# Optimization experiments

Hardware: AMD Instinct MI355X
Metric: run time of the kernel (lower is better)

Reference implementation:

```python
import jax, jax.numpy as jnp
import numpy as np

B = 8192          # batch of agents
K = 4             # max_neighbors
NUM_LANES = 12
LANE_F = 4        # obs_dim // num_lanes = 48 // 12
HEADS = 4
OUT = 32          # gat_output_dim per head
EMB = HEADS * OUT # 128, gat_per_lane_output / intersection emb dim
HID = 64          # graphsage_hidden_dim
GRU_H = 32        # gru_hidden_dim
ALPHA = 0.2       # leaky relu slope

# Lane cooperation: lanes of the same approach (4 approaches x 3 lanes) cooperate.
_blk = np.kron(np.eye(4), np.ones((3, 3))).astype(np.float32)
LANE_COOP = jnp.asarray(_blk)
LANE_CONF = jnp.asarray(1.0 - _blk)


def _gat_stream(x, W, a_src, a_dst, adj):
    # x: [N, 12, 4]; W: [H, 4, O]; a_*: [H, O]; adj: [12, 12]
    Wh = jnp.einsum('nlf,hfo->nhlo', x, W)                      # [N,H,12,O]
    e_s = jnp.einsum('nhlo,ho->nhl', Wh, a_src)
    e_d = jnp.einsum('nhlo,ho->nhl', Wh, a_dst)
    e = jax.nn.leaky_relu(e_s[..., :, None] + e_d[..., None, :], ALPHA)  # [N,H,12,12]
    e = jnp.where(adj[None, None] > 0, e, jnp.float32(-1e9))
    att = jax.nn.softmax(e, axis=-1)
    out = jnp.einsum('nhij,nhjo->niho', att, Wh)                # [N,12,H,O]
    return jax.nn.elu(out.reshape(out.shape[0], NUM_LANES, EMB))


def _gru_final(xs, Wih, Whh, bih, bhh):
    # xs: [K, B, HID] -> final hidden [B, GRU_H], torch GRU gate convention (r,z,n)
    def step(h, x):
        gi = x @ Wih + bih
        gh = h @ Whh + bhh
        i_r, i_z, i_n = jnp.split(gi, 3, axis=-1)
        h_r, h_z, h_n = jnp.split(gh, 3, axis=-1)
        r = jax.nn.sigmoid(i_r + h_r)
        z = jax.nn.sigmoid(i_z + h_z)
        n = jnp.tanh(i_n + r * h_n)
        return (1.0 - z) * n + z * h, None
    h0 = jnp.zeros((xs.shape[1], Whh.shape[0]), xs.dtype)
    hT, _ = jax.lax.scan(step, h0, xs)
    return hT


def setup_inputs() -> dict:
    key = jax.random.key(0)
    ks = jax.random.split(key, 24)
    rn = lambda k, s: (jax.random.normal(k, s, jnp.float32) * 0.1)
    z = lambda n: jnp.zeros((n,), jnp.float32)
    return {
        'self_features': jax.random.normal(ks[0], (B, 48), jnp.float32),
        'neighbor_features': jax.random.normal(ks[1], (B, K, 48), jnp.float32),
        'neighbor_mask': (jax.random.uniform(ks[2], (B, K)) > 0.25).astype(jnp.float32),
        'neighbor_directions': jax.random.randint(ks[3], (B, K), 0, 4).astype(jnp.float32) * 0.25,
        # dual-stream GAT params
        'W_coop': rn(ks[4], (HEADS, LANE_F, OUT)), 'a_src_coop': rn(ks[5], (HEADS, OUT)), 'a_dst_coop': rn(ks[6], (HEADS, OUT)),
        'W_conf': rn(ks[7], (HEADS, LANE_F, OUT)), 'a_src_conf': rn(ks[8], (HEADS, OUT)), 'a_dst_conf': rn(ks[9], (HEADS, OUT)),
        'W_fuse': rn(ks[10], (2 * EMB, EMB)), 'b_fuse': z(EMB),
        # GraphSAGE neighbor projection (+1 for direction feature)
        'W_proj': rn(ks[11], (EMB + 1, HID)), 'b_proj': z(HID),
        # BiGRU (fwd/bwd), torch layout transposed: Wih [HID,3H], Whh [H,3H]
        'Wih_f': rn(ks[12], (HID, 3 * GRU_H)), 'Whh_f': rn(ks[13], (GRU_H, 3 * GRU_H)), 'bih_f': z(3 * GRU_H), 'bhh_f': z(3 * GRU_H),
        'Wih_b': rn(ks[14], (HID, 3 * GRU_H)), 'Whh_b': rn(ks[15], (GRU_H, 3 * GRU_H)), 'bih_b': z(3 * GRU_H), 'bhh_b': z(3 * GRU_H),
        # combine self + BiGRU summary -> network embedding
        'W_out': rn(ks[16], (EMB + 2 * GRU_H, HID)), 'b_out': z(HID),
    }


def reference(self_features, neighbor_features, neighbor_mask, neighbor_directions,
              W_coop, a_src_coop, a_dst_coop, W_conf, a_src_conf, a_dst_conf,
              W_fuse, b_fuse, W_proj, b_proj,
              Wih_f, Whh_f, bih_f, bhh_f, Wih_b, Whh_b, bih_b, bhh_b,
              W_out, b_out):
    Bc, Kc = neighbor_features.shape[:2]
    # run dual-stream GAT on self + all neighbors in one batch of small lane graphs
    allx = jnp.concatenate([self_features[:, None, :], neighbor_features], axis=1)
    allx = allx.reshape(Bc * (Kc + 1), NUM_LANES, LANE_F)
    coop = _gat_stream(allx, W_coop, a_src_coop, a_dst_coop, LANE_COOP)
    conf = _gat_stream(allx, W_conf, a_src_conf, a_dst_conf, LANE_CONF)
    fused = jax.nn.elu(jnp.concatenate([coop, conf], axis=-1) @ W_fuse + b_fuse)  # [N,12,128]
    emb = fused.mean(axis=1).reshape(Bc, Kc + 1, EMB)  # mean pool over lanes
    self_emb = emb[:, 0]          # [B,128]
    nbr_emb = emb[:, 1:]          # [B,K,128]
    # GraphSAGE projection of neighbors (direction-aware), masked
    nbr_in = jnp.concatenate([nbr_emb, neighbor_directions[..., None]], axis=-1)
    x = jax.nn.relu(nbr_in @ W_proj + b_proj) * neighbor_mask[..., None]  # [B,K,HID]
    xs = jnp.swapaxes(x, 0, 1)    # [K,B,HID]
    h_f = _gru_final(xs, Wih_f, Whh_f, bih_f, bhh_f)
    h_b = _gru_final(xs[::-1], Wih_b, Whh_b, bih_b, bhh_b)
    net = jax.nn.relu(jnp.concatenate([self_emb, h_f, h_b], axis=-1) @ W_out + b_out)  # [B,64]
    return jnp.concatenate([self_emb, net], axis=-1)  # [B,192]
```

## Files before the change

kernel.cpp:

```cpp
#include <hip/hip_runtime.h>
#include <math.h>

typedef short short8 __attribute__((ext_vector_type(8)));
typedef float f32x4  __attribute__((ext_vector_type(4)));
typedef unsigned short u16x4 __attribute__((ext_vector_type(4)));

__device__ __forceinline__ unsigned short f2b(float f) {
  union { float f; unsigned int u; } x; x.f = f;
  return (unsigned short)((x.u + 0x7FFFu + ((x.u >> 16) & 1u)) >> 16);
}
__device__ __forceinline__ float b2f_u(unsigned short u) {
  union { unsigned int u; float f; } x; x.u = ((unsigned int)u) << 16;
  return x.f;
}
__device__ __forceinline__ float sigm(float x) { return 1.f / (1.f + __expf(-x)); }

__global__ __launch_bounds__(256) void prepack_kernel(
    const float* __restrict__ Wf,
    const float* __restrict__ Wc, const float* __restrict__ Wn,
    const float* __restrict__ as_c, const float* __restrict__ ad_c,
    const float* __restrict__ as_n, const float* __restrict__ ad_n,
    const float* __restrict__ Wproj,
    const float* __restrict__ Wih_f, const float* __restrict__ Wih_b,
    const float* __restrict__ Wout,
    const float* __restrict__ Whh_f, const float* __restrict__ Whh_b,
    unsigned short* __restrict__ fragB,
    unsigned short* __restrict__ fragWB,
    float* __restrict__ Wa,
    unsigned short* __restrict__ fragP,
    unsigned short* __restrict__ fragIH,
    unsigned short* __restrict__ fragO,
    unsigned short* __restrict__ fragHH)
{
  int e = blockIdx.x * 256 + threadIdx.x;
  unsigned short tmp[8];
  if (e < 4096) {
    int kb = e >> 9, tile = (e >> 6) & 7, lane = e & 63;
    int n = tile * 16 + (lane & 15);
    int kbase = kb * 32 + (lane >> 4) * 8;
#pragma unroll
    for (int j = 0; j < 8; j++) tmp[j] = f2b(Wf[(kbase + j) * 128 + n]);
    *(short8*)(fragB + e * 8) = *(short8*)tmp;
  } else if (e < 5120) {
    int i = e - 4096;
    int s = i >> 9, tile = (i >> 6) & 7, lane = i & 63;
    int c15 = lane & 15, quad = lane >> 4;
    int n = tile * 16 + c15;
    int h = n >> 5, o = n & 31;
    const float* W = s ? Wn : Wc;
#pragma unroll
    for (int j = 0; j < 8; j++) {
      int k = quad * 8 + j;
      tmp[j] = ((k >> 2) == h) ? f2b(W[h * 128 + (k & 3) * 32 + o])
                               : (unsigned short)0;
    }
    *(short8*)(fragWB + i * 8) = *(short8*)tmp;
  } else if (e < 5184) {
    int i = e - 5120;
    int s = i >> 5, d = (i >> 4) & 1, h = (i >> 2) & 3, f = i & 3;
    const float* W = s ? Wn : Wc;
    const float* a = s ? (d ? ad_n : as_n) : (d ? ad_c : as_c);
    float acc = 0.f;
#pragma unroll
    for (int o = 0; o < 32; o++) acc += W[h * 128 + f * 32 + o] * a[h * 32 + o];
    Wa[i] = acc;
  } else if (e < 6208) {
    int i = e - 5184;
    int kb = i >> 8, nt = (i >> 6) & 3, lane = i & 63;
    int c15 = lane & 15, quad = lane >> 4;
#pragma unroll
    for (int j = 0; j < 8; j++)
      tmp[j] = f2b(Wproj[(kb * 32 + quad * 8 + j) * 64 + nt * 16 + c15]);
    *(short8*)(fragP + i * 8) = *(short8*)tmp;
  } else if (e < 7744) {
    int i = e - 6208;
    int d = (i >= 768), r = i - d * 768;
    int kb = r / 384, nt = (r >> 6) % 6, lane = r & 63;
    int c15 = lane & 15, quad = lane >> 4;
    const float* W = d ? Wih_b : Wih_f;
#pragma unroll
    for (int j = 0; j < 8; j++)
      tmp[j] = f2b(W[(kb * 32 + quad * 8 + j) * 96 + nt * 16 + c15]);
    *(short8*)(fragIH + i * 8) = *(short8*)tmp;
  } else if (e < 9280) {
    int r = e - 7744;
    int kb = r >> 8, nt = (r >> 6) & 3, lane = r & 63;
    int c15 = lane & 15, quad = lane >> 4;
#pragma unroll
    for (int j = 0; j < 8; j++)
      tmp[j] = f2b(Wout[(kb * 32 + quad * 8 + j) * 64 + nt * 16 + c15]);
    *(short8*)(fragO + r * 8) = *(short8*)tmp;
  } else if (e < 10048) {
    int i = e - 9280;
    int d = i / 384, r = i - d * 384;
    int nt = r >> 6, lane = r & 63;
    int c15 = lane & 15, quad = lane >> 4;
    const float* W = d ? Whh_b : Whh_f;
#pragma unroll
    for (int j = 0; j < 8; j++)
      tmp[j] = f2b(W[(quad * 8 + j) * 96 + nt * 16 + c15]);
    *(short8*)(fragHH + i * 8) = *(short8*)tmp;
  }
}

__global__ __launch_bounds__(256) void gat_fuse_kernel(
    const float* __restrict__ self_f, const float* __restrict__ nbr_f,
    const float* __restrict__ Wa,
    const unsigned short* __restrict__ fragWB,
    const unsigned short* __restrict__ fragB,
    const float* __restrict__ b_fuse,
    float* __restrict__ emb)
{
  const int tid = threadIdx.x;
  const int w = tid >> 6, lane = tid & 63, c15 = lane & 15, quad = lane >> 4;
  const int n0 = blockIdx.x * 2;
  const int ws = w & 1;
  const int wn = w >> 1;

  __shared__ __align__(16) float sxf[2][12][4];
  __shared__ float sWa[64];
  __shared__ float sed[2][2][4][12];
  __shared__ __align__(16) unsigned short sA[2][2][16][24];
  __shared__ __align__(16) unsigned short scatb[2][16][268];
  __shared__ float sbias[128];

  if (tid < 128) sbias[tid] = b_fuse[tid];
  if (tid < 64) sWa[tid] = Wa[tid];
  if (tid < 96) {
    int nd = tid / 48, f = tid - nd * 48;
    int nn = n0 + nd, b = nn / 5, slot = nn - b * 5;
    float v = (slot == 0) ? self_f[b * 48 + f]
                          : nbr_f[(b * 4 + slot - 1) * 48 + f];
    sxf[nd][f >> 2][f & 3] = v;
  }
  __syncthreads();

  float es_local = 0.f;
  if (tid < 192) {
    int g = tid / 96, r = tid - g * 96;
    int s = r / 48, r2 = r - s * 48;
    int h = r2 / 12, l = r2 - h * 12;
    float ed = 0.f;
#pragma unroll
    for (int f = 0; f < 4; f++) {
      float xv = sxf[g][l][f];
      es_local += xv * sWa[s * 32 + h * 4 + f];
      ed       += xv * sWa[s * 32 + 16 + h * 4 + f];
    }
    sed[g][s][h][l] = ed;
  }
  __syncthreads();

  if (tid < 192) {
    int g = tid / 96, r = tid - g * 96;
    int s = r / 48, r2 = r - s * 48;
    int h = r2 / 12, i = r2 - h * 12;
    int blk = i / 3;
    float ev[12];
    float m = -1e30f;
#pragma unroll
    for (int j = 0; j < 12; j++) {
      bool allowed = (s == 0) ? ((j / 3) == blk) : ((j / 3) != blk);
      float e = es_local + sed[g][s][h][j];
      e = e > 0.f ? e : 0.2f * e;
      if (!allowed) e = -1e30f;
      ev[j] = e;
      m = fmaxf(m, e);
    }
    float sum = 0.f;
#pragma unroll
    for (int j = 0; j < 12; j++) {
      float a = (ev[j] > -1e29f) ? __expf(ev[j] - m) : 0.f;
      ev[j] = a;
      sum += a;
    }
    float inv = 1.f / sum;
    float xa0 = 0.f, xa1 = 0.f, xa2 = 0.f, xa3 = 0.f;
#pragma unroll
    for (int j = 0; j < 12; j++) {
      float aj = ev[j] * inv;
      f32x4 xj = *(const f32x4*)&sxf[g][j][0];
      xa0 += aj * xj[0]; xa1 += aj * xj[1];
      xa2 += aj * xj[2]; xa3 += aj * xj[3];
    }
    u16x4 pk = { f2b(xa0), f2b(xa1), f2b(xa2), f2b(xa3) };
    *(u16x4*)&sA[g][s][i][h * 4] = pk;
  }
  __syncthreads();

  {
    const short8 z8 = {0,0,0,0,0,0,0,0};
    short8 a = z8;
    if (quad < 2) a = *(const short8*)&sA[wn][ws][c15][quad * 8];
#pragma unroll
    for (int tile = 0; tile < 8; tile++) {
      short8 bw = *(const short8*)(fragWB + ((ws * 8 + tile) * 64 + lane) * 8);
      f32x4 c = {0.f, 0.f, 0.f, 0.f};
      c = __builtin_amdgcn_mfma_f32_16x16x32_bf16(a, bw, c, 0, 0, 0);
      if (quad < 3) {
        int co = ws * 128 + tile * 16 + c15;
#pragma unroll
        for (int r = 0; r < 4; r++) {
          float v = c[r];
          v = v > 0.f ? v : (__expf(v) - 1.f);
          scatb[wn][quad * 4 + r][co] = f2b(v);
        }
      }
    }
  }
  __syncthreads();

  {
    f32x4 acc[2][2];
#pragma unroll
    for (int nd = 0; nd < 2; nd++)
#pragma unroll
      for (int tt = 0; tt < 2; tt++) acc[nd][tt] = (f32x4){0.f,0.f,0.f,0.f};
#pragma unroll
    for (int kb = 0; kb < 8; kb++) {
      short8 a0 = *(const short8*)&scatb[0][c15][kb * 32 + (quad << 3)];
      short8 a1 = *(const short8*)&scatb[1][c15][kb * 32 + (quad << 3)];
#pragma unroll
      for (int tt = 0; tt < 2; tt++) {
        short8 bw = *(const short8*)(fragB + ((kb * 8 + 2 * w + tt) * 64 + lane) * 8);
        acc[0][tt] = __builtin_amdgcn_mfma_f32_16x16x32_bf16(a0, bw, acc[0][tt], 0, 0, 0);
        acc[1][tt] = __builtin_amdgcn_mfma_f32_16x16x32_bf16(a1, bw, acc[1][tt], 0, 0, 0);
      }
    }
    float tot[2][2];
#pragma unroll
    for (int nd = 0; nd < 2; nd++) {
#pragma unroll
      for (int tt = 0; tt < 2; tt++) {
        float p = 0.f;
        if (quad < 3) {
          float bcol = sbias[w * 32 + tt * 16 + c15];
#pragma unroll
          for (int r = 0; r < 4; r++) {
            float v = acc[nd][tt][r] + bcol;
            v = v > 0.f ? v : (__expf(v) - 1.f);
            p += v;
          }
        }
        p += __shfl_xor(p, 16);
        p += __shfl_xor(p, 32);
        tot[nd][tt] = p;
      }
    }
    int ndw = quad >> 1, ttw = quad & 1;
    float val = ndw ? (ttw ? tot[1][1] : tot[1][0])
                    : (ttw ? tot[0][1] : tot[0][0]);
    emb[(n0 + ndw) * 128 + w * 32 + ttw * 16 + c15] = val * (1.f / 12.f);
  }
}

__global__ __launch_bounds__(256) void head_kernel(
    const float* __restrict__ emb,
    const float* __restrict__ maskp, const float* __restrict__ dirsp,
    const float* __restrict__ W_proj, const float* __restrict__ b_proj,
    const unsigned short* __restrict__ fragP,
    const unsigned short* __restrict__ fragIH,
    const unsigned short* __restrict__ fragHH,
    const float* __restrict__ bih_f, const float* __restrict__ bhh_f,
    const float* __restrict__ bih_b, const float* __restrict__ bhh_b,
    const unsigned short* __restrict__ fragO,
    const float* __restrict__ b_out,
    float* __restrict__ out)
{
  const int b8 = blockIdx.x * 8;
  const int tid = threadIdx.x;
  const int w = tid >> 6, lane = tid & 63, c15 = lane & 15, quad = lane >> 4;

  __shared__ __align__(16) unsigned short sX[32][72];
  __shared__ __align__(16) unsigned short sgi[2][32][96];
  __shared__ float sH[2][8][32];
  __shared__ __align__(16) unsigned short sHb[2][16][32];
  __shared__ float sgh[2][8][96];
  __shared__ __align__(16) unsigned short sCat[16][200];
  __shared__ float sPB[128];
  __shared__ float sBI[2][96], sBH[2][96], sBO[64];

  if (tid < 64) { sPB[tid] = b_proj[tid]; sPB[64 + tid] = W_proj[128 * 64 + tid]; sBO[tid] = b_out[tid]; }
  if (tid < 96) { sBI[0][tid] = bih_f[tid]; sBI[1][tid] = bih_b[tid];
                  sBH[0][tid] = bhh_f[tid]; sBH[1][tid] = bhh_b[tid]; }
  {
    unsigned int* hb = (unsigned int*)sHb;
    hb[tid] = 0u; hb[tid + 256] = 0u;
    float* hz = (float*)sH;
    for (int i = tid; i < 512; i += 256) hz[i] = 0.f;
  }
  __syncthreads();

  {
    const int mt = w >> 1;
    const int nt0 = (w & 1) * 2;
    const int sloc = mt * 4 + (c15 >> 2);
    const int nbr  = c15 & 3;
    const float* arow = emb + (((b8 + sloc) * 5) + 1 + nbr) * 128;
    short8 a[4];
#pragma unroll
    for (int kb = 0; kb < 4; kb++) {
      const float* p = arow + kb * 32 + quad * 8;
      f32x4 v0 = *(const f32x4*)p;
      f32x4 v1 = *(const f32x4*)(p + 4);
      unsigned short tmp[8];
      tmp[0]=f2b(v0[0]); tmp[1]=f2b(v0[1]); tmp[2]=f2b(v0[2]); tmp[3]=f2b(v0[3]);
      tmp[4]=f2b(v1[0]); tmp[5]=f2b(v1[1]); tmp[6]=f2b(v1[2]); tmp[7]=f2b(v1[3]);
      a[kb] = *(short8*)tmp;
    }
    f32x4 acc0 = {0.f,0.f,0.f,0.f}, acc1 = acc0;
#pragma unroll
    for (int kb = 0; kb < 4; kb++) {
      short8 b0 = *(const short8*)(fragP + ((kb * 4 + nt0    ) * 64 + lane) * 8);
      short8 b1 = *(const short8*)(fragP + ((kb * 4 + nt0 + 1) * 64 + lane) * 8);
      acc0 = __builtin_amdgcn_mfma_f32_16x16x32_bf16(a[kb], b0, acc0, 0, 0, 0);
      acc1 = __builtin_amdgcn_mfma_f32_16x16x32_bf16(a[kb], b1, acc1, 0, 0, 0);
    }
    const int sE = mt * 4 + quad;
    float dirv[4], maskv[4];
#pragma unroll
    for (int r = 0; r < 4; r++) {
      dirv[r]  = dirsp[(b8 + sE) * 4 + r];
      maskv[r] = maskp[(b8 + sE) * 4 + r];
    }
#pragma unroll
    for (int tt = 0; tt < 2; tt++) {
      f32x4 c = tt ? acc1 : acc0;
      int col = (nt0 + tt) * 16 + c15;
#pragma unroll
      for (int r = 0; r < 4; r++) {
        float v = c[r] + dirv[r] * sPB[64 + col] + sPB[col];
        v = fmaxf(v, 0.f) * maskv[r];
        sX[mt * 16 + quad * 4 + r][col] = f2b(v);
      }
    }
  }
  __syncthreads();

  {
    const int mt = w >> 1;
    const int ntb = (w & 1) * 3;
    short8 a[2];
#pragma unroll
    for (int kb = 0; kb < 2; kb++)
      a[kb] = *(const short8*)&sX[mt * 16 + c15][kb * 32 + quad * 8];
#pragma unroll
    for (int d = 0; d < 2; d++) {
#pragma unroll
      for (int t2 = 0; t2 < 3; t2++) {
        int nt = ntb + t2;
        f32x4 acc = {0.f,0.f,0.f,0.f};
#pragma unroll
        for (int kb = 0; kb < 2; kb++) {
          short8 bb = *(const short8*)(fragIH + ((d * 12 + kb * 6 + nt) * 64 + lane) * 8);
          acc = __builtin_amdgcn_mfma_f32_16x16x32_bf16(a[kb], bb, acc, 0, 0, 0);
        }
        int col = nt * 16 + c15;
        float bi = sBI[d][col];
#pragma unroll
        for (int r = 0; r < 4; r++)
          sgi[d][mt * 16 + quad * 4 + r][col] = f2b(acc[r] + bi);
      }
    }
  }
  __syncthreads();

  {
    const int d_mfma = w >> 1;
    const int nt0 = (w & 1) * 3;
    const int u = tid & 31;
    const int s = (tid >> 5) & 7;
    const int grow = s * 4;
    for (int step = 0; step < 4; step++) {
      short8 a = *(const short8*)&sHb[d_mfma][c15][quad * 8];
#pragma unroll
      for (int t2 = 0; t2 < 3; t2++) {
        short8 bb = *(const short8*)(fragHH + ((d_mfma * 6 + nt0 + t2) * 64 + lane) * 8);
        f32x4 c = {0.f,0.f,0.f,0.f};
        c = __builtin_amdgcn_mfma_f32_16x16x32_bf16(a, bb, c, 0, 0, 0);
        if (quad < 2) {
          int col = (nt0 + t2) * 16 + c15;
#pragma unroll
          for (int r = 0; r < 4; r++)
            sgh[d_mfma][quad * 4 + r][col] = c[r];
        }
      }
      __syncthreads();
#pragma unroll
      for (int d = 0; d < 2; d++) {
        int k = d ? (3 - step) : step;
        int row = grow + k;
        float ghr = sgh[d][s][u]      + sBH[d][u];
        float ghz = sgh[d][s][32 + u] + sBH[d][32 + u];
        float ghn = sgh[d][s][64 + u] + sBH[d][64 + u];
        float r = sigm(b2f_u(sgi[d][row][u]) + ghr);
        float z = sigm(b2f_u(sgi[d][row][32 + u]) + ghz);
        float n = tanhf(b2f_u(sgi[d][row][64 + u]) + r * ghn);
        float h = (1.f - z) * n + z * sH[d][s][u];
        sH[d][s][u] = h;
        sHb[d][s][u] = f2b(h);
      }
      __syncthreads();
    }
  }

  for (int i = tid; i < 8 * 128; i += 256) {
    int s = i >> 7, cc = i & 127;
    sCat[s][cc] = f2b(emb[(b8 + s) * 5 * 128 + cc]);
  }
  for (int i = tid; i < 512; i += 256) {
    int s = i >> 6, j = i & 63;
    float hv = (j < 32) ? sH[0][s][j] : sH[1][s][j - 32];
    sCat[s][128 + j] = f2b(hv);
  }
  __syncthreads();

  {
    const int nt = w;
    f32x4 acc = {0.f,0.f,0.f,0.f};
#pragma unroll
    for (int kb = 0; kb < 6; kb++) {
      short8 a = *(const short8*)&sCat[c15][kb * 32 + quad * 8];
      short8 bb = *(const short8*)(fragO + ((kb * 4 + nt) * 64 + lane) * 8);
      acc = __builtin_amdgcn_mfma_f32_16x16x32_bf16(a, bb, acc, 0, 0, 0);
    }
    if (quad < 2) {
      int col = nt * 16 + c15;
#pragma unroll
      for (int r = 0; r < 4; r++) {
        int m = quad * 4 + r;
        out[(b8 + m) * 192 + 128 + col] = fmaxf(acc[r] + sBO[col], 0.f);
      }
    }
  }
  for (int i = tid; i < 8 * 128; i += 256) {
    int s = i >> 7, cc = i & 127;
    out[(b8 + s) * 192 + cc] = emb[(b8 + s) * 5 * 128 + cc];
  }
}

extern "C" void kernel_launch(void* const* d_in, const int* in_sizes, int n_in,
                              void* d_out, int out_size, void* d_ws, size_t ws_size,
                              hipStream_t stream) {
  const float* self_f  = (const float*)d_in[0];
  const float* nbr_f   = (const float*)d_in[1];
  const float* maskp   = (const float*)d_in[2];
  const float* dirsp   = (const float*)d_in[3];
  const float* W_coop  = (const float*)d_in[4];
  const float* as_coop = (const float*)d_in[5];
  const float* ad_coop = (const float*)d_in[6];
  const float* W_conf  = (const float*)d_in[7];
  const float* as_conf = (const float*)d_in[8];
  const float* ad_conf = (const float*)d_in[9];
  const float* W_fuse  = (const float*)d_in[10];
  const float* b_fuse  = (const float*)d_in[11];
  const float* W_proj  = (const float*)d_in[12];
  const float* b_proj  = (const float*)d_in[13];
  const float* Wih_f   = (const float*)d_in[14];
  const float* Whh_f   = (const float*)d_in[15];
  const float* bih_f   = (const float*)d_in[16];
  const float* bhh_f   = (const float*)d_in[17];
  const float* Wih_b   = (const float*)d_in[18];
  const float* Whh_b   = (const float*)d_in[19];
  const float* bih_b   = (const float*)d_in[20];
  const float* bhh_b   = (const float*)d_in[21];
  const float* W_out   = (const float*)d_in[22];
  const float* b_out   = (const float*)d_in[23];

  const int B = in_sizes[0] / 48;
  char* ws = (char*)d_ws;
  unsigned short* fragB  = (unsigned short*)(ws);
  unsigned short* fragWB = (unsigned short*)(ws + 65536);
  float*          Wa     = (float*)(ws + 81920);
  unsigned short* fragP  = (unsigned short*)(ws + 82176);
  unsigned short* fragIH = (unsigned short*)(ws + 98560);
  unsigned short* fragO  = (unsigned short*)(ws + 123136);
  unsigned short* fragHH = (unsigned short*)(ws + 147712);
  float*          emb    = (float*)(ws + 160000);

  prepack_kernel<<<40, 256, 0, stream>>>(
      W_fuse, W_coop, W_conf, as_coop, ad_coop, as_conf, ad_conf,
      W_proj, Wih_f, Wih_b, W_out, Whh_f, Whh_b,
      fragB, fragWB, Wa, fragP, fragIH, fragO, fragHH);

  gat_fuse_kernel<<<B * 5 / 2, 256, 0, stream>>>(
      self_f, nbr_f, Wa, fragWB, fragB, b_fuse, emb);

  head_kernel<<<B / 8, 256, 0, stream>>>(
      emb, maskp, dirsp, W_proj, b_proj, fragP, fragIH, fragHH,
      bih_f, bhh_f, bih_b, bhh_b,
      fragO, b_out, (float*)d_out);
}
```

Measured before the change: 239.3 us.

## Shrink head kernel to 4 agents per block with per-wave GRU direction

The head kernel now handles 4 agents per 128-thread block instead of 8 per 256-thread block. Each wave owns one GRU direction end to end, so the two block-wide barriers per recurrent step can be dropped. LDS buffers are shrunk and aliased, and tanhf is replaced by an exp-based fast tanh. The launch now has twice as many blocks, and the MFMA tiles are underused since only 4 of 16 rows hold data.

```diff
diff --git a/kernel.cpp b/kernel.cpp
--- a/kernel.cpp
+++ b/kernel.cpp
@@ -14,6 +14,10 @@
   return x.f;
 }
 __device__ __forceinline__ float sigm(float x) { return 1.f / (1.f + __expf(-x)); }
+__device__ __forceinline__ float tanh_fast(float x) {
+  float t = __expf(2.f * x);
+  return 1.f - 2.f / (t + 1.f);
+}
 
 __global__ __launch_bounds__(256) void prepack_kernel(
     const float* __restrict__ Wf,
@@ -254,7 +258,7 @@
   }
 }
 
-__global__ __launch_bounds__(256) void head_kernel(
+__global__ __launch_bounds__(128) void head_kernel(
     const float* __restrict__ emb,
     const float* __restrict__ maskp, const float* __restrict__ dirsp,
     const float* __restrict__ W_proj, const float* __restrict__ b_proj,
@@ -267,36 +271,35 @@
     const float* __restrict__ b_out,
     float* __restrict__ out)
 {
-  const int b8 = blockIdx.x * 8;
+  const int b4 = blockIdx.x * 4;
   const int tid = threadIdx.x;
   const int w = tid >> 6, lane = tid & 63, c15 = lane & 15, quad = lane >> 4;
 
-  __shared__ __align__(16) unsigned short sX[32][72];
-  __shared__ __align__(16) unsigned short sgi[2][32][96];
-  __shared__ float sH[2][8][32];
+  __shared__ __align__(16) unsigned short sXC[16][200];
+  __shared__ __align__(16) unsigned short sgi[2][16][96];
+  __shared__ float sH[2][4][32];
   __shared__ __align__(16) unsigned short sHb[2][16][32];
-  __shared__ float sgh[2][8][96];
-  __shared__ __align__(16) unsigned short sCat[16][200];
+  __shared__ float sgh[2][4][96];
   __shared__ float sPB[128];
   __shared__ float sBI[2][96], sBH[2][96], sBO[64];
+
+  unsigned short (*sX)[72] = (unsigned short(*)[72])&sXC[0][0];
 
   if (tid < 64) { sPB[tid] = b_proj[tid]; sPB[64 + tid] = W_proj[128 * 64 + tid]; sBO[tid] = b_out[tid]; }
   if (tid < 96) { sBI[0][tid] = bih_f[tid]; sBI[1][tid] = bih_b[tid];
                   sBH[0][tid] = bhh_f[tid]; sBH[1][tid] = bhh_b[tid]; }
   {
     unsigned int* hb = (unsigned int*)sHb;
-    hb[tid] = 0u; hb[tid + 256] = 0u;
+#pragma unroll
+    for (int i = 0; i < 4; i++) hb[tid + 128 * i] = 0u;
     float* hz = (float*)sH;
-    for (int i = tid; i < 512; i += 256) hz[i] = 0.f;
-  }
-  __syncthreads();
-
-  {
-    const int mt = w >> 1;
-    const int nt0 = (w & 1) * 2;
-    const int sloc = mt * 4 + (c15 >> 2);
-    const int nbr  = c15 & 3;
-    const float* arow = emb + (((b8 + sloc) * 5) + 1 + nbr) * 128;
+    hz[tid] = 0.f; hz[tid + 128] = 0.f;
+  }
+  __syncthreads();
+
+  {
+    const int sl = c15 >> 2, nbr = c15 & 3;
+    const float* arow = emb + (((b4 + sl) * 5) + 1 + nbr) * 128;
     short8 a[4];
 #pragma unroll
     for (int kb = 0; kb < 4; kb++) {
@@ -308,134 +311,124 @@
       tmp[4]=f2b(v1[0]); tmp[5]=f2b(v1[1]); tmp[6]=f2b(v1[2]); tmp[7]=f2b(v1[3]);
       a[kb] = *(short8*)tmp;
     }
-    f32x4 acc0 = {0.f,0.f,0.f,0.f}, acc1 = acc0;
-#pragma unroll
-    for (int kb = 0; kb < 4; kb++) {
-      short8 b0 = *(const short8*)(fragP + ((kb * 4 + nt0    ) * 64 + lane) * 8);
-      short8 b1 = *(const short8*)(fragP + ((kb * 4 + nt0 + 1) * 64 + lane) * 8);
-      acc0 = __builtin_amdgcn_mfma_f32_16x16x32_bf16(a[kb], b0, acc0, 0, 0, 0);
-      acc1 = __builtin_amdgcn_mfma_f32_16x16x32_bf16(a[kb], b1, acc1, 0, 0, 0);
-    }
-    const int sE = mt * 4 + quad;
     float dirv[4], maskv[4];
 #pragma unroll
     for (int r = 0; r < 4; r++) {
-      dirv[r]  = dirsp[(b8 + sE) * 4 + r];
-      maskv[r] = maskp[(b8 + sE) * 4 + r];
+      dirv[r]  = dirsp[(b4 + quad) * 4 + r];
+      maskv[r] = maskp[(b4 + quad) * 4 + r];
     }
 #pragma unroll
     for (int tt = 0; tt < 2; tt++) {
-      f32x4 c = tt ? acc1 : acc0;
-      int col = (nt0 + tt) * 16 + c15;
+      int nt = w * 2 + tt;
+      f32x4 acc = {0.f,0.f,0.f,0.f};
+#pragma unroll
+      for (int kb = 0; kb < 4; kb++) {
+        short8 bb = *(const short8*)(fragP + ((kb * 4 + nt) * 64 + lane) * 8);
+        acc = __builtin_amdgcn_mfma_f32_16x16x32_bf16(a[kb], bb, acc, 0, 0, 0);
+      }
+      int col = nt * 16 + c15;
 #pragma unroll
       for (int r = 0; r < 4; r++) {
-        float v = c[r] + dirv[r] * sPB[64 + col] + sPB[col];
+        float v = acc[r] + dirv[r] * sPB[64 + col] + sPB[col];
         v = fmaxf(v, 0.f) * maskv[r];
-        sX[mt * 16 + quad * 4 + r][col] = f2b(v);
-      }
-    }
-  }
-  __syncthreads();
-
-  {
-    const int mt = w >> 1;
-    const int ntb = (w & 1) * 3;
+        sX[quad * 4 + r][col] = f2b(v);
+      }
+    }
+  }
+  __syncthreads();
+
+  {
+    const int d = w;
     short8 a[2];
 #pragma unroll
     for (int kb = 0; kb < 2; kb++)
-      a[kb] = *(const short8*)&sX[mt * 16 + c15][kb * 32 + quad * 8];
-#pragma unroll
-    for (int d = 0; d < 2; d++) {
-#pragma unroll
-      for (int t2 = 0; t2 < 3; t2++) {
-        int nt = ntb + t2;
-        f32x4 acc = {0.f,0.f,0.f,0.f};
-#pragma unroll
-        for (int kb = 0; kb < 2; kb++) {
-          short8 bb = *(const short8*)(fragIH + ((d * 12 + kb * 6 + nt) * 64 + lane) * 8);
-          acc = __builtin_amdgcn_mfma_f32_16x16x32_bf16(a[kb], bb, acc, 0, 0, 0);
-        }
-        int col = nt * 16 + c15;
-        float bi = sBI[d][col];
-#pragma unroll
-        for (int r = 0; r < 4; r++)
-          sgi[d][mt * 16 + quad * 4 + r][col] = f2b(acc[r] + bi);
-      }
-    }
-  }
-  __syncthreads();
-
-  {
-    const int d_mfma = w >> 1;
-    const int nt0 = (w & 1) * 3;
-    const int u = tid & 31;
-    const int s = (tid >> 5) & 7;
-    const int grow = s * 4;
+      a[kb] = *(const short8*)&sX[c15][kb * 32 + quad * 8];
+#pragma unroll
+    for (int nt = 0; nt < 6; nt++) {
+      f32x4 acc = {0.f,0.f,0.f,0.f};
+#pragma unroll
+      for (int kb = 0; kb < 2; kb++) {
+        short8 bb = *(const short8*)(fragIH + ((d * 12 + kb * 6 + nt) * 64 + lane) * 8);
+        acc = __builtin_amdgcn_mfma_f32_16x16x32_bf16(a[kb], bb, acc, 0, 0, 0);
+      }
+      int col = nt * 16 + c15;
+      float bi = sBI[d][col];
+#pragma unroll
+      for (int r = 0; r < 4; r++)
+        sgi[d][quad * 4 + r][col] = f2b(acc[r] + bi);
+    }
+  }
+  __syncthreads();
+
+  {
+    const int d = w;
+    const int u = lane & 31;
+    const int s0 = (lane >> 5) ? 1 : 0;
     for (int step = 0; step < 4; step++) {
-      short8 a = *(const short8*)&sHb[d_mfma][c15][quad * 8];
-#pragma unroll
-      for (int t2 = 0; t2 < 3; t2++) {
-        short8 bb = *(const short8*)(fragHH + ((d_mfma * 6 + nt0 + t2) * 64 + lane) * 8);
+      short8 a = *(const short8*)&sHb[d][c15][quad * 8];
+#pragma unroll
+      for (int nt = 0; nt < 6; nt++) {
+        short8 bb = *(const short8*)(fragHH + ((d * 6 + nt) * 64 + lane) * 8);
         f32x4 c = {0.f,0.f,0.f,0.f};
         c = __builtin_amdgcn_mfma_f32_16x16x32_bf16(a, bb, c, 0, 0, 0);
-        if (quad < 2) {
-          int col = (nt0 + t2) * 16 + c15;
-#pragma unroll
-          for (int r = 0; r < 4; r++)
-            sgh[d_mfma][quad * 4 + r][col] = c[r];
+        if (quad == 0) {
+          int col = nt * 16 + c15;
+#pragma unroll
+          for (int r = 0; r < 4; r++) sgh[d][r][col] = c[r];
         }
       }
-      __syncthreads();
-#pragma unroll
-      for (int d = 0; d < 2; d++) {
-        int k = d ? (3 - step) : step;
-        int row = grow + k;
+      const int k = d ? (3 - step) : step;
+#pragma unroll
+      for (int si = 0; si < 2; si++) {
+        int s = s0 + si * 2;
+        int row = s * 4 + k;
         float ghr = sgh[d][s][u]      + sBH[d][u];
         float ghz = sgh[d][s][32 + u] + sBH[d][32 + u];
         float ghn = sgh[d][s][64 + u] + sBH[d][64 + u];
         float r = sigm(b2f_u(sgi[d][row][u]) + ghr);
         float z = sigm(b2f_u(sgi[d][row][32 + u]) + ghz);
-        float n = tanhf(b2f_u(sgi[d][row][64 + u]) + r * ghn);
+        float n = tanh_fast(b2f_u(sgi[d][row][64 + u]) + r * ghn);
         float h = (1.f - z) * n + z * sH[d][s][u];
         sH[d][s][u] = h;
         sHb[d][s][u] = f2b(h);
       }
-      __syncthreads();
-    }
-  }
-
-  for (int i = tid; i < 8 * 128; i += 256) {
+    }
+  }
+  __syncthreads();
+
+  for (int i = tid; i < 512; i += 128) {
     int s = i >> 7, cc = i & 127;
-    sCat[s][cc] = f2b(emb[(b8 + s) * 5 * 128 + cc]);
-  }
-  for (int i = tid; i < 512; i += 256) {
+    sXC[s][cc] = f2b(emb[(b4 + s) * 5 * 128 + cc]);
+  }
+  for (int i = tid; i < 256; i += 128) {
     int s = i >> 6, j = i & 63;
     float hv = (j < 32) ? sH[0][s][j] : sH[1][s][j - 32];
-    sCat[s][128 + j] = f2b(hv);
-  }
-  __syncthreads();
-
-  {
-    const int nt = w;
-    f32x4 acc = {0.f,0.f,0.f,0.f};
-#pragma unroll
-    for (int kb = 0; kb < 6; kb++) {
-      short8 a = *(const short8*)&sCat[c15][kb * 32 + quad * 8];
-      short8 bb = *(const short8*)(fragO + ((kb * 4 + nt) * 64 + lane) * 8);
-      acc = __builtin_amdgcn_mfma_f32_16x16x32_bf16(a, bb, acc, 0, 0, 0);
-    }
-    if (quad < 2) {
-      int col = nt * 16 + c15;
-#pragma unroll
-      for (int r = 0; r < 4; r++) {
-        int m = quad * 4 + r;
-        out[(b8 + m) * 192 + 128 + col] = fmaxf(acc[r] + sBO[col], 0.f);
-      }
-    }
-  }
-  for (int i = tid; i < 8 * 128; i += 256) {
+    sXC[s][128 + j] = f2b(hv);
+  }
+  __syncthreads();
+
+  {
+#pragma unroll
+    for (int tt = 0; tt < 2; tt++) {
+      int nt = w * 2 + tt;
+      f32x4 acc = {0.f,0.f,0.f,0.f};
+#pragma unroll
+      for (int kb = 0; kb < 6; kb++) {
+        short8 a = *(const short8*)&sXC[c15][kb * 32 + quad * 8];
+        short8 bb = *(const short8*)(fragO + ((kb * 4 + nt) * 64 + lane) * 8);
+        acc = __builtin_amdgcn_mfma_f32_16x16x32_bf16(a, bb, acc, 0, 0, 0);
+      }
+      if (quad == 0) {
+        int col = nt * 16 + c15;
+#pragma unroll
+        for (int r = 0; r < 4; r++)
+          out[(b4 + r) * 192 + 128 + col] = fmaxf(acc[r] + sBO[col], 0.f);
+      }
+    }
+  }
+  for (int i = tid; i < 512; i += 128) {
     int s = i >> 7, cc = i & 127;
-    out[(b8 + s) * 192 + cc] = emb[(b8 + s) * 5 * 128 + cc];
+    out[(b4 + s) * 192 + cc] = emb[(b4 + s) * 5 * 128 + cc];
   }
 }
 
@@ -486,7 +479,7 @@
   gat_fuse_kernel<<<B * 5 / 2, 256, 0, stream>>>(
       self_f, nbr_f, Wa, fragWB, fragB, b_fuse, emb);
 
-  head_kernel<<<B / 8, 256, 0, stream>>>(
+  head_kernel<<<B / 4, 128, 0, stream>>>(
       emb, maskp, dirsp, W_proj, b_proj, fragP, fragIH, fragHH,
       bih_f, bhh_f, bih_b, bhh_b,
       fragO, b_out, (float*)d_out);
```

Measured after the change: 246.3 us. 2.9% more time.
